# Kernel tuning notes

Hardware: AMD Instinct MI355X
Metric: run time of the kernel (lower is better)

## Reference

```python
import jax, jax.numpy as jnp
import numpy as np

D_MODEL = 1024
N_HEADS = 16
HEAD_DIM = D_MODEL // N_HEADS
D_FF = 4096
WINDOW = 128
LN_EPS = 1e-5
NEG_INF = jnp.finfo(jnp.float32).min


def layer_norm(x, w, b):
    mu = jnp.mean(x, axis=-1, keepdims=True)
    var = jnp.mean(jnp.square(x - mu), axis=-1, keepdims=True)
    return (x - mu) * jax.lax.rsqrt(var + LN_EPS) * w + b


def setup_inputs() -> dict:
    key = jax.random.key(0)
    ks = jax.random.split(key, 12)
    B, L, D = 2, 2048, D_MODEL
    s = 1.0 / np.sqrt(D)
    inp = {
        "x": jax.random.normal(ks[0], (B, L, D), jnp.float32),
        "Wq": jax.random.normal(ks[1], (D, D), jnp.float32) * s,
        "bq": jnp.zeros((D,), jnp.float32),
        "Wk": jax.random.normal(ks[2], (D, D), jnp.float32) * s,
        "bk": jnp.zeros((D,), jnp.float32),
        "Wv": jax.random.normal(ks[3], (D, D), jnp.float32) * s,
        "bv": jnp.zeros((D,), jnp.float32),
        "Wo": jax.random.normal(ks[4], (D, D), jnp.float32) * s,
        "bo": jnp.zeros((D,), jnp.float32),
        "W1": jax.random.normal(ks[5], (D, D_FF), jnp.float32) * s,
        "b1": jnp.zeros((D_FF,), jnp.float32),
        "W2": jax.random.normal(ks[6], (D_FF, D), jnp.float32) * (1.0 / np.sqrt(D_FF)),
        "b2": jnp.zeros((D,), jnp.float32),
        "ln1_w": jnp.ones((D,), jnp.float32),
        "ln1_b": jnp.zeros((D,), jnp.float32),
        "ln2_w": jnp.ones((D,), jnp.float32),
        "ln2_b": jnp.zeros((D,), jnp.float32),
    }
    return inp


def reference(x, Wq, bq, Wk, bk, Wv, bv, Wo, bo, W1, b1, W2, b2,
              ln1_w, ln1_b, ln2_w, ln2_b):
    B, L, D = x.shape
    # causal sliding-window additive bias: allow j <= i and i - j <= WINDOW
    i = jnp.arange(L)[:, None]
    j = jnp.arange(L)[None, :]
    band = (j > i) | ((i - j) > WINDOW)          # [L, L] True = masked
    bias = jnp.where(band, NEG_INF, 0.0).astype(x.dtype)  # [L, L]

    # --- attention sub-block (pre-LN) ---
    h = layer_norm(x, ln1_w, ln1_b)
    q = (h @ Wq + bq).reshape(B, L, N_HEADS, HEAD_DIM)
    k = (h @ Wk + bk).reshape(B, L, N_HEADS, HEAD_DIM)
    v = (h @ Wv + bv).reshape(B, L, N_HEADS, HEAD_DIM)
    scale = 1.0 / np.sqrt(HEAD_DIM)
    scores = jnp.einsum("blhd,bmhd->bhlm", q, k) * scale + bias  # [B,H,L,L]
    attn = jax.nn.softmax(scores, axis=-1)
    ctx = jnp.einsum("bhlm,bmhd->blhd", attn, v).reshape(B, L, D)
    x = x + ctx @ Wo + bo

    # --- FFN sub-block (pre-LN, GELU) ---
    h2 = layer_norm(x, ln2_w, ln2_b)
    x = x + jax.nn.gelu(h2 @ W1 + b1) @ W2 + b2
    return x
```

## Files before the change

kernel.cpp:

```cpp
#include <hip/hip_runtime.h>

#define DMODEL 1024
#define NHEADS 16
#define HDIM 64
#define DFF 4096
#define WINDOW 128
#define LROWS 2048
#define BATCH 2
#define MROWS (BATCH*LROWS)

typedef __attribute__((ext_vector_type(8))) __bf16 bf16x8;
typedef __attribute__((ext_vector_type(4))) float f32x4;

typedef const __attribute__((address_space(1))) void* gp1;
typedef __attribute__((address_space(3))) void* lp3;

__device__ inline unsigned short f2bf(float f) {
  union { float f; unsigned int u; } c; c.f = f;
  unsigned int u = c.u;
  unsigned int r = (u + 0x7fffu + ((u >> 16) & 1u)) >> 16;
  return (unsigned short)r;
}
__device__ inline float bf2f(unsigned short s) {
  union { unsigned int u; float f; } c; c.u = ((unsigned int)s) << 16;
  return c.f;
}

__global__ __launch_bounds__(256)
void transpose_bf16(const float* __restrict__ in, unsigned short* __restrict__ out,
                    int R, int C) {
  __shared__ float tile[32][33];
  const int c0 = blockIdx.x * 32, r0 = blockIdx.y * 32;
  const int tx = threadIdx.x, ty = threadIdx.y;
  #pragma unroll
  for (int r = 0; r < 4; ++r) {
    int rr = ty + r * 8;
    tile[rr][tx] = in[(size_t)(r0 + rr) * C + c0 + tx];
  }
  __syncthreads();
  #pragma unroll
  for (int r = 0; r < 4; ++r) {
    int rr = ty + r * 8;
    out[(size_t)(c0 + rr) * R + r0 + tx] = f2bf(tile[tx][rr]);
  }
}

__global__ __launch_bounds__(256)
void concat_bias(const float* __restrict__ a, const float* __restrict__ b,
                 const float* __restrict__ c, float* __restrict__ o) {
  const int i = blockIdx.x * 256 + threadIdx.x;
  float v = (i < 1024) ? a[i] : (i < 2048) ? b[i - 1024] : c[i - 2048];
  o[i] = v;
}

__global__ __launch_bounds__(256)
void ln_kernel(const float* __restrict__ x, const float* __restrict__ w,
               const float* __restrict__ b, unsigned short* __restrict__ out) {
  const int row = blockIdx.x;
  const int tid = threadIdx.x;
  const float4 v = *(const float4*)(x + (size_t)row * DMODEL + tid * 4);
  float s = v.x + v.y + v.z + v.w;
  float sq = v.x * v.x + v.y * v.y + v.z * v.z + v.w * v.w;
  #pragma unroll
  for (int off = 32; off; off >>= 1) {
    s += __shfl_xor(s, off);
    sq += __shfl_xor(sq, off);
  }
  __shared__ float rs_[4], rq_[4];
  const int lane = tid & 63, wid = tid >> 6;
  if (lane == 0) { rs_[wid] = s; rq_[wid] = sq; }
  __syncthreads();
  s = rs_[0] + rs_[1] + rs_[2] + rs_[3];
  sq = rq_[0] + rq_[1] + rq_[2] + rq_[3];
  const float mean = s * (1.0f / DMODEL);
  const float var = sq * (1.0f / DMODEL) - mean * mean;
  const float rstd = rsqrtf(var + 1e-5f);
  const float4 wv = *(const float4*)(w + tid * 4);
  const float4 bv = *(const float4*)(b + tid * 4);
  ushort4 o;
  o.x = f2bf((v.x - mean) * rstd * wv.x + bv.x);
  o.y = f2bf((v.y - mean) * rstd * wv.y + bv.y);
  o.z = f2bf((v.z - mean) * rstd * wv.z + bv.z);
  o.w = f2bf((v.w - mean) * rstd * wv.w + bv.w);
  *(ushort4*)(out + (size_t)row * DMODEL + tid * 4) = o;
}

template<int ACT, bool RES, bool OUTBF>
__global__ __launch_bounds__(256)
void gemm_kernel(const unsigned short* __restrict__ A, const unsigned short* __restrict__ Bt,
                 const float* __restrict__ bias, const float* __restrict__ resid,
                 void* __restrict__ outp, int N, int K) {
  __shared__ __align__(16) unsigned short lda[128 * 64];
  __shared__ __align__(16) unsigned short ldb[128 * 64];
  const int tid = threadIdx.x;
  const int lane = tid & 63;
  const int wid = tid >> 6;
  const int wm = (wid >> 1) * 64;
  const int wn = (wid & 1) * 64;
  const int m0 = blockIdx.y * 128;
  const int n0 = blockIdx.x * 128;

  f32x4 acc[4][4];
  #pragma unroll
  for (int mi = 0; mi < 4; ++mi)
    #pragma unroll
    for (int nj = 0; nj < 4; ++nj)
      acc[mi][nj] = (f32x4){0.f, 0.f, 0.f, 0.f};

  const int src_inner = ((lane & 7) << 4) ^ ((lane >> 3) << 4);
  const int rbase = wid * 32 + (lane >> 3);
  const char* gA0 = (const char*)(A + (size_t)(m0 + rbase) * K) + src_inner;
  const char* gB0 = (const char*)(Bt + (size_t)(n0 + rbase) * K) + src_inner;
  const size_t rowstep = (size_t)8 * K * 2;

  for (int kt = 0; kt < K; kt += 64) {
    const size_t koff = (size_t)kt * 2;
    #pragma unroll
    for (int r = 0; r < 4; ++r) {
      __builtin_amdgcn_global_load_lds((gp1)(gA0 + r * rowstep + koff),
                                       (lp3)((char*)lda + (wid * 4 + r) * 1024), 16, 0, 0);
      __builtin_amdgcn_global_load_lds((gp1)(gB0 + r * rowstep + koff),
                                       (lp3)((char*)ldb + (wid * 4 + r) * 1024), 16, 0, 0);
    }
    __syncthreads();
    #pragma unroll
    for (int kk = 0; kk < 2; ++kk) {
      bf16x8 af[4], bfr[4];
      #pragma unroll
      for (int mi = 0; mi < 4; ++mi) {
        const int row = wm + mi * 16 + (lane & 15);
        const int off = (row * 128 + kk * 64 + (lane >> 4) * 16) ^ ((row & 7) << 4);
        af[mi] = *(const bf16x8*)((const char*)lda + off);
      }
      #pragma unroll
      for (int nj = 0; nj < 4; ++nj) {
        const int row = wn + nj * 16 + (lane & 15);
        const int off = (row * 128 + kk * 64 + (lane >> 4) * 16) ^ ((row & 7) << 4);
        bfr[nj] = *(const bf16x8*)((const char*)ldb + off);
      }
      #pragma unroll
      for (int mi = 0; mi < 4; ++mi)
        #pragma unroll
        for (int nj = 0; nj < 4; ++nj)
          acc[mi][nj] = __builtin_amdgcn_mfma_f32_16x16x32_bf16(af[mi], bfr[nj], acc[mi][nj], 0, 0, 0);
    }
    __syncthreads();
  }

  #pragma unroll
  for (int mi = 0; mi < 4; ++mi) {
    #pragma unroll
    for (int nj = 0; nj < 4; ++nj) {
      const int col = n0 + wn + nj * 16 + (lane & 15);
      const float bc = bias[col];
      const int rbase2 = m0 + wm + mi * 16 + ((lane >> 4) << 2);
      #pragma unroll
      for (int r = 0; r < 4; ++r) {
        const size_t idx = (size_t)(rbase2 + r) * N + col;
        float v = acc[mi][nj][r] + bc;
        if (ACT == 1) {
          const float x3 = v * v * v;
          v = 0.5f * v * (1.0f + tanhf(0.7978845608028654f * (v + 0.044715f * x3)));
        }
        if (RES) v += resid[idx];
        if (OUTBF) ((unsigned short*)outp)[idx] = f2bf(v);
        else       ((float*)outp)[idx] = v;
      }
    }
  }
}

#define KSPAN 192
#define VPITCH 200

__global__ __launch_bounds__(256)
void attn_kernel(const unsigned short* __restrict__ QKV, unsigned short* __restrict__ O) {
  __shared__ __align__(16) unsigned short k_lds[KSPAN * 64];
  __shared__ __align__(16) unsigned short vt_lds[64 * VPITCH];
  const int tid = threadIdx.x;
  const int lane = tid & 63;
  const int w = tid >> 6;
  const int m = lane & 15;
  const int g = lane >> 4;

  const int qb = blockIdx.x & 31;
  const int h  = (blockIdx.x >> 5) & 15;
  const int b  = blockIdx.x >> 9;
  const int i0 = qb * 64;

  const size_t rowp = 3 * DMODEL;
  const size_t base = (size_t)b * LROWS * rowp;

  for (int it = 0; it < 6; ++it) {
    const int c = tid + it * 256;
    const int kk = c >> 3, dc = c & 7;
    int krow = i0 - 128 + kk; krow = krow < 0 ? 0 : krow;
    const unsigned short* src = QKV + base + (size_t)krow * rowp + DMODEL + h * HDIM + dc * 8;
    const uint4 kv = *(const uint4*)src;
    const int koff = (kk * 128 + dc * 16) ^ (((kk >> 1) & 7) << 4);
    *(uint4*)((char*)k_lds + koff) = kv;
    union { uint4 v; unsigned short s[8]; } u; u.v = *(const uint4*)(src + DMODEL);
    #pragma unroll
    for (int j = 0; j < 8; ++j)
      vt_lds[(dc * 8 + j) * VPITCH + kk] = u.s[j];
  }
  __syncthreads();

  const int qrow = i0 + 16 * w + m;
  const unsigned short* qptr = QKV + base + (size_t)qrow * rowp + h * HDIM + g * 8;
  const bf16x8 qf0 = *(const bf16x8*)qptr;
  const bf16x8 qf1 = *(const bf16x8*)(qptr + 32);

  const int q_rel = 16 * w + m;
  const int lo128 = 128 - i0;
  const int qlo = lo128 > q_rel ? lo128 : q_rel;
  const int qhi = q_rel + 128;
  const int offw = (w < 2) ? 16 * w : 32;

  float sc[5][2][4];
  #pragma unroll
  for (int c5 = 0; c5 < 5; ++c5) {
    const int key0 = offw + c5 * 32;
    f32x4 a0 = {0.f, 0.f, 0.f, 0.f}, a1 = {0.f, 0.f, 0.f, 0.f};
    const int kre = key0 + 2 * m;
    const int sl = (m & 7) << 4;
    const bf16x8 ke0 = *(const bf16x8*)((const char*)k_lds + ((kre * 128 + g * 16) ^ sl));
    const bf16x8 ke1 = *(const bf16x8*)((const char*)k_lds + ((kre * 128 + 64 + g * 16) ^ sl));
    a0 = __builtin_amdgcn_mfma_f32_16x16x32_bf16(ke0, qf0, a0, 0, 0, 0);
    a0 = __builtin_amdgcn_mfma_f32_16x16x32_bf16(ke1, qf1, a0, 0, 0, 0);
    const bf16x8 ko0 = *(const bf16x8*)((const char*)k_lds + (((kre + 1) * 128 + g * 16) ^ sl));
    const bf16x8 ko1 = *(const bf16x8*)((const char*)k_lds + (((kre + 1) * 128 + 64 + g * 16) ^ sl));
    a1 = __builtin_amdgcn_mfma_f32_16x16x32_bf16(ko0, qf0, a1, 0, 0, 0);
    a1 = __builtin_amdgcn_mfma_f32_16x16x32_bf16(ko1, qf1, a1, 0, 0, 0);
    #pragma unroll
    for (int r = 0; r < 4; ++r) {
      const int je = key0 + 8 * g + 2 * r;
      sc[c5][0][r] = (je >= qlo && je <= qhi) ? a0[r] * 0.125f : -1e30f;
      const int jo = je + 1;
      sc[c5][1][r] = (jo >= qlo && jo <= qhi) ? a1[r] * 0.125f : -1e30f;
    }
  }

  float mx = -1e30f;
  #pragma unroll
  for (int c5 = 0; c5 < 5; ++c5)
    #pragma unroll
    for (int t = 0; t < 2; ++t)
      #pragma unroll
      for (int r = 0; r < 4; ++r) mx = fmaxf(mx, sc[c5][t][r]);
  mx = fmaxf(mx, __shfl_xor(mx, 16));
  mx = fmaxf(mx, __shfl_xor(mx, 32));
  float sum = 0.f;
  #pragma unroll
  for (int c5 = 0; c5 < 5; ++c5)
    #pragma unroll
    for (int t = 0; t < 2; ++t)
      #pragma unroll
      for (int r = 0; r < 4; ++r) {
        const float p = __expf(sc[c5][t][r] - mx);
        sc[c5][t][r] = p;
        sum += p;
      }
  sum += __shfl_xor(sum, 16);
  sum += __shfl_xor(sum, 32);
  const float rden = 1.0f / sum;

  f32x4 oacc[4];
  #pragma unroll
  for (int dt = 0; dt < 4; ++dt) oacc[dt] = (f32x4){0.f, 0.f, 0.f, 0.f};
  #pragma unroll
  for (int c5 = 0; c5 < 5; ++c5) {
    union { bf16x8 v; unsigned short s[8]; } yu;
    #pragma unroll
    for (int r = 0; r < 4; ++r) {
      yu.s[2 * r]     = f2bf(sc[c5][0][r]);
      yu.s[2 * r + 1] = f2bf(sc[c5][1][r]);
    }
    const int key0 = offw + c5 * 32;
    #pragma unroll
    for (int dt = 0; dt < 4; ++dt) {
      const bf16x8 vf = *(const bf16x8*)(vt_lds + (dt * 16 + m) * VPITCH + key0 + 8 * g);
      oacc[dt] = __builtin_amdgcn_mfma_f32_16x16x32_bf16(vf, yu.v, oacc[dt], 0, 0, 0);
    }
  }

  unsigned short* orow = O + (size_t)(b * LROWS + i0 + 16 * w + m) * DMODEL + h * HDIM;
  #pragma unroll
  for (int dt = 0; dt < 4; ++dt)
    #pragma unroll
    for (int r = 0; r < 4; ++r)
      orow[dt * 16 + 4 * g + r] = f2bf(oacc[dt][r] * rden);
}

extern "C" void kernel_launch(void* const* d_in, const int* in_sizes, int n_in,
                              void* d_out, int out_size, void* d_ws, size_t ws_size,
                              hipStream_t stream) {
  const float* x    = (const float*)d_in[0];
  const float* Wq   = (const float*)d_in[1];
  const float* bq   = (const float*)d_in[2];
  const float* Wk   = (const float*)d_in[3];
  const float* bk   = (const float*)d_in[4];
  const float* Wv   = (const float*)d_in[5];
  const float* bv   = (const float*)d_in[6];
  const float* Wo   = (const float*)d_in[7];
  const float* bo   = (const float*)d_in[8];
  const float* W1   = (const float*)d_in[9];
  const float* b1   = (const float*)d_in[10];
  const float* W2   = (const float*)d_in[11];
  const float* b2   = (const float*)d_in[12];
  const float* ln1w = (const float*)d_in[13];
  const float* ln1b = (const float*)d_in[14];
  const float* ln2w = (const float*)d_in[15];
  const float* ln2b = (const float*)d_in[16];

  char* ws = (char*)d_ws;
  const size_t MB = 1024ull * 1024ull;
  unsigned short* Wqkvt = (unsigned short*)(ws + 0 * MB);
  unsigned short* Wot   = (unsigned short*)(ws + 6 * MB);
  unsigned short* W1t   = (unsigned short*)(ws + 8 * MB);
  unsigned short* W2t   = (unsigned short*)(ws + 16 * MB);
  float*          bqkv  = (float*)(ws + 24 * MB);
  unsigned short* QKV   = (unsigned short*)(ws + 25 * MB);
  unsigned short* H1    = (unsigned short*)(ws + 49 * MB);
  unsigned short* CTX   = (unsigned short*)(ws + 49 * MB);
  unsigned short* H2    = (unsigned short*)(ws + 0 * MB);
  unsigned short* FFN1  = (unsigned short*)(ws + 25 * MB);

  dim3 tb(32, 8);
  transpose_bf16<<<dim3(32, 32), tb, 0, stream>>>(Wq, Wqkvt, DMODEL, DMODEL);
  transpose_bf16<<<dim3(32, 32), tb, 0, stream>>>(Wk, Wqkvt + 1024 * 1024, DMODEL, DMODEL);
  transpose_bf16<<<dim3(32, 32), tb, 0, stream>>>(Wv, Wqkvt + 2048 * 1024, DMODEL, DMODEL);
  transpose_bf16<<<dim3(32, 32), tb, 0, stream>>>(Wo, Wot, DMODEL, DMODEL);
  transpose_bf16<<<dim3(128, 32), tb, 0, stream>>>(W1, W1t, DMODEL, DFF);
  transpose_bf16<<<dim3(32, 128), tb, 0, stream>>>(W2, W2t, DFF, DMODEL);
  concat_bias<<<12, 256, 0, stream>>>(bq, bk, bv, bqkv);

  ln_kernel<<<MROWS, 256, 0, stream>>>(x, ln1w, ln1b, H1);

  gemm_kernel<0, false, true><<<dim3(24, 32), 256, 0, stream>>>(H1, Wqkvt, bqkv, nullptr, QKV, 3 * DMODEL, DMODEL);

  attn_kernel<<<BATCH * NHEADS * (LROWS / 64), 256, 0, stream>>>(QKV, CTX);

  gemm_kernel<0, true, false><<<dim3(8, 32), 256, 0, stream>>>(CTX, Wot, bo, x, d_out, DMODEL, DMODEL);

  ln_kernel<<<MROWS, 256, 0, stream>>>((const float*)d_out, ln2w, ln2b, H2);

  gemm_kernel<1, false, true><<<dim3(32, 32), 256, 0, stream>>>(H2, W1t, b1, nullptr, FFN1, DFF, DMODEL);

  gemm_kernel<0, true, false><<<dim3(8, 32), 256, 0, stream>>>(FFN1, W2t, b2, (const float*)d_out, d_out, DMODEL, DFF);
}
```

Measured before the change: 366.7 us.

## Double-buffer GEMM LDS tiles and use 64-row tiles for N=1024 GEMMs

The GEMM kernel now uses two LDS buffers and issues the global-to-LDS loads for the next K tile before computing on the current one, so memory latency can overlap with MFMA work. The M tile size becomes a template parameter, and the two N=1024 GEMMs (output projection and FFN down-projection) use 64-row tiles, doubling their grid from 256 to 512 blocks to fill more CUs. The costs are doubled LDS per block, which may reduce occupancy, and less reuse per block for the smaller tiles.

```diff
diff --git a/kernel.cpp b/kernel.cpp
--- a/kernel.cpp
+++ b/kernel.cpp
@@ -85,70 +85,81 @@
   *(ushort4*)(out + (size_t)row * DMODEL + tid * 4) = o;
 }
 
-template<int ACT, bool RES, bool OUTBF>
+template<int BM, int ACT, bool RES, bool OUTBF>
 __global__ __launch_bounds__(256)
 void gemm_kernel(const unsigned short* __restrict__ A, const unsigned short* __restrict__ Bt,
                  const float* __restrict__ bias, const float* __restrict__ resid,
                  void* __restrict__ outp, int N, int K) {
-  __shared__ __align__(16) unsigned short lda[128 * 64];
-  __shared__ __align__(16) unsigned short ldb[128 * 64];
+  constexpr int MI = BM / 32;
+  constexpr int RA = BM / 32;
+  __shared__ __align__(16) unsigned short lda[2][BM * 64];
+  __shared__ __align__(16) unsigned short ldb[2][128 * 64];
   const int tid = threadIdx.x;
   const int lane = tid & 63;
   const int wid = tid >> 6;
-  const int wm = (wid >> 1) * 64;
+  const int wm = (wid >> 1) * (BM / 2);
   const int wn = (wid & 1) * 64;
-  const int m0 = blockIdx.y * 128;
+  const int m0 = blockIdx.y * BM;
   const int n0 = blockIdx.x * 128;
 
-  f32x4 acc[4][4];
-  #pragma unroll
-  for (int mi = 0; mi < 4; ++mi)
+  f32x4 acc[MI][4];
+  #pragma unroll
+  for (int mi = 0; mi < MI; ++mi)
     #pragma unroll
     for (int nj = 0; nj < 4; ++nj)
       acc[mi][nj] = (f32x4){0.f, 0.f, 0.f, 0.f};
 
   const int src_inner = ((lane & 7) << 4) ^ ((lane >> 3) << 4);
-  const int rbase = wid * 32 + (lane >> 3);
-  const char* gA0 = (const char*)(A + (size_t)(m0 + rbase) * K) + src_inner;
-  const char* gB0 = (const char*)(Bt + (size_t)(n0 + rbase) * K) + src_inner;
+  const int rbaseA = wid * (BM / 4) + (lane >> 3);
+  const int rbaseB = wid * 32 + (lane >> 3);
+  const char* gA0 = (const char*)(A + (size_t)(m0 + rbaseA) * K) + src_inner;
+  const char* gB0 = (const char*)(Bt + (size_t)(n0 + rbaseB) * K) + src_inner;
   const size_t rowstep = (size_t)8 * K * 2;
 
+  auto stage = [&](int buf, int kt) {
+    const size_t koff = (size_t)kt * 2;
+    #pragma unroll
+    for (int r = 0; r < RA; ++r)
+      __builtin_amdgcn_global_load_lds((gp1)(gA0 + r * rowstep + koff),
+                                       (lp3)((char*)lda[buf] + (wid * RA + r) * 1024), 16, 0, 0);
+    #pragma unroll
+    for (int r = 0; r < 4; ++r)
+      __builtin_amdgcn_global_load_lds((gp1)(gB0 + r * rowstep + koff),
+                                       (lp3)((char*)ldb[buf] + (wid * 4 + r) * 1024), 16, 0, 0);
+  };
+
+  stage(0, 0);
+  __syncthreads();
+  int cur = 0;
   for (int kt = 0; kt < K; kt += 64) {
-    const size_t koff = (size_t)kt * 2;
-    #pragma unroll
-    for (int r = 0; r < 4; ++r) {
-      __builtin_amdgcn_global_load_lds((gp1)(gA0 + r * rowstep + koff),
-                                       (lp3)((char*)lda + (wid * 4 + r) * 1024), 16, 0, 0);
-      __builtin_amdgcn_global_load_lds((gp1)(gB0 + r * rowstep + koff),
-                                       (lp3)((char*)ldb + (wid * 4 + r) * 1024), 16, 0, 0);
-    }
-    __syncthreads();
+    if (kt + 64 < K) stage(cur ^ 1, kt + 64);
     #pragma unroll
     for (int kk = 0; kk < 2; ++kk) {
-      bf16x8 af[4], bfr[4];
-      #pragma unroll
-      for (int mi = 0; mi < 4; ++mi) {
+      bf16x8 af[MI], bfr[4];
+      #pragma unroll
+      for (int mi = 0; mi < MI; ++mi) {
         const int row = wm + mi * 16 + (lane & 15);
         const int off = (row * 128 + kk * 64 + (lane >> 4) * 16) ^ ((row & 7) << 4);
-        af[mi] = *(const bf16x8*)((const char*)lda + off);
+        af[mi] = *(const bf16x8*)((const char*)lda[cur] + off);
       }
       #pragma unroll
       for (int nj = 0; nj < 4; ++nj) {
         const int row = wn + nj * 16 + (lane & 15);
         const int off = (row * 128 + kk * 64 + (lane >> 4) * 16) ^ ((row & 7) << 4);
-        bfr[nj] = *(const bf16x8*)((const char*)ldb + off);
+        bfr[nj] = *(const bf16x8*)((const char*)ldb[cur] + off);
       }
       #pragma unroll
-      for (int mi = 0; mi < 4; ++mi)
+      for (int mi = 0; mi < MI; ++mi)
         #pragma unroll
         for (int nj = 0; nj < 4; ++nj)
           acc[mi][nj] = __builtin_amdgcn_mfma_f32_16x16x32_bf16(af[mi], bfr[nj], acc[mi][nj], 0, 0, 0);
     }
     __syncthreads();
-  }
-
-  #pragma unroll
-  for (int mi = 0; mi < 4; ++mi) {
+    cur ^= 1;
+  }
+
+  #pragma unroll
+  for (int mi = 0; mi < MI; ++mi) {
     #pragma unroll
     for (int nj = 0; nj < 4; ++nj) {
       const int col = n0 + wn + nj * 16 + (lane & 15);
@@ -337,15 +348,15 @@
 
   ln_kernel<<<MROWS, 256, 0, stream>>>(x, ln1w, ln1b, H1);
 
-  gemm_kernel<0, false, true><<<dim3(24, 32), 256, 0, stream>>>(H1, Wqkvt, bqkv, nullptr, QKV, 3 * DMODEL, DMODEL);
+  gemm_kernel<128, 0, false, true><<<dim3(24, 32), 256, 0, stream>>>(H1, Wqkvt, bqkv, nullptr, QKV, 3 * DMODEL, DMODEL);
 
   attn_kernel<<<BATCH * NHEADS * (LROWS / 64), 256, 0, stream>>>(QKV, CTX);
 
-  gemm_kernel<0, true, false><<<dim3(8, 32), 256, 0, stream>>>(CTX, Wot, bo, x, d_out, DMODEL, DMODEL);
+  gemm_kernel<64, 0, true, false><<<dim3(8, 64), 256, 0, stream>>>(CTX, Wot, bo, x, d_out, DMODEL, DMODEL);
 
   ln_kernel<<<MROWS, 256, 0, stream>>>((const float*)d_out, ln2w, ln2b, H2);
 
-  gemm_kernel<1, false, true><<<dim3(32, 32), 256, 0, stream>>>(H2, W1t, b1, nullptr, FFN1, DFF, DMODEL);
-
-  gemm_kernel<0, true, false><<<dim3(8, 32), 256, 0, stream>>>(FFN1, W2t, b2, (const float*)d_out, d_out, DMODEL, DFF);
-}
+  gemm_kernel<128, 1, false, true><<<dim3(32, 32), 256, 0, stream>>>(H2, W1t, b1, nullptr, FFN1, DFF, DMODEL);
+
+  gemm_kernel<64, 0, true, false><<<dim3(8, 64), 256, 0, stream>>>(FFN1, W2t, b2, (const float*)d_out, d_out, DMODEL, DFF);
+}
```

After: 336.7 us. -8.2%, faster.
